# Optimization experiments

Measured on AMD Instinct MI355X. Metric: run time of the kernel, lower is better.

The kernel has to match this reference:

```python
import jax, jax.numpy as jnp
import numpy as np

N_NODES = 100000
N_EDGES = 1600000
EMBED = 64
HEADS = 8
HEAD_DIM = EMBED // HEADS
FFN = 4 * EMBED
EPS = 1e-5


def _layer_norm(x, g, b):
    m = jnp.mean(x, axis=-1, keepdims=True)
    v = jnp.mean(jnp.square(x - m), axis=-1, keepdims=True)
    return (x - m) * jax.lax.rsqrt(v + EPS) * g + b


def setup_inputs() -> dict:
    key = jax.random.key(0)
    ks = jax.random.split(key, 10)
    s = lambda fan_in: 1.0 / np.sqrt(fan_in)
    x = jax.random.normal(ks[0], (N_NODES, EMBED), dtype=jnp.float32)
    edge_indices = jax.random.randint(ks[1], (2, N_EDGES), 0, N_NODES, dtype=jnp.int64)
    attn_w = jax.random.uniform(ks[2], (EMBED, 3 * EMBED), jnp.float32, -s(EMBED), s(EMBED))
    attn_b = jnp.zeros((3 * EMBED,), jnp.float32)
    w1 = jax.random.uniform(ks[3], (EMBED, FFN), jnp.float32, -s(EMBED), s(EMBED))
    b1 = jnp.zeros((FFN,), jnp.float32)
    w2 = jax.random.uniform(ks[4], (FFN, EMBED), jnp.float32, -s(FFN), s(FFN))
    b2 = jnp.zeros((EMBED,), jnp.float32)
    ln1_g = jnp.ones((EMBED,), jnp.float32)
    ln1_b = jnp.zeros((EMBED,), jnp.float32)
    ln2_g = jnp.ones((EMBED,), jnp.float32)
    ln2_b = jnp.zeros((EMBED,), jnp.float32)
    return {"x": x, "edge_indices": edge_indices, "attn_w": attn_w, "attn_b": attn_b,
            "w1": w1, "b1": b1, "w2": w2, "b2": b2,
            "ln1_g": ln1_g, "ln1_b": ln1_b, "ln2_g": ln2_g, "ln2_b": ln2_b}


def _self_attention(x, edge_indices, attn_w, attn_b):
    n = x.shape[0]
    row, col = edge_indices[0], edge_indices[1]
    scale = EMBED ** (-0.5)  # note: original scales by embed_dim**-0.5
    qkv = (x @ attn_w + attn_b).reshape(n, HEADS, 3 * HEAD_DIM)
    q, k, v = jnp.split(qkv, 3, axis=2)  # each [N, H, Dh]
    alpha = jnp.sum(q[row] * k[col], axis=2) * scale  # [E, H]
    # sparse per-row softmax via segment reductions
    m = jax.ops.segment_max(alpha, row, num_segments=n)  # [N, H]
    e = jnp.exp(alpha - m[row])
    denom = jax.ops.segment_sum(e, row, num_segments=n)  # [N, H]
    weights = e / denom[row]  # [E, H]
    vals = v[col] * weights[:, :, None]  # [E, H, Dh]
    out = jax.ops.segment_sum(vals, row, num_segments=n)  # [N, H, Dh]
    return out.reshape(n, EMBED)


def reference(x, edge_indices, attn_w, attn_b, w1, b1, w2, b2, ln1_g, ln1_b, ln2_g, ln2_b):
    # post-norm (norm_first=False), dropout=0
    x = _layer_norm(x + _self_attention(x, edge_indices, attn_w, attn_b), ln1_g, ln1_b)
    ffn = jax.nn.relu(x @ w1 + b1) @ w2 + b2
    x = _layer_norm(x + ffn, ln2_g, ln2_b)
    return x
```

## Files before the change

kernel.cpp:

```cpp
#include <hip/hip_runtime.h>
#include <hip/hip_bf16.h>
#include <hip/hip_fp8.h>


#define WAVE 64
constexpr int BUCKET_SHIFT = 7;
constexpr int NBMAX = 800;

typedef __attribute__((ext_vector_type(8))) short bf16x8;
typedef __attribute__((ext_vector_type(4))) float f32x4;
typedef __attribute__((ext_vector_type(2))) float f32x2;

union BF8 {
  bf16x8 v;
  unsigned u[4];
};

__device__ __forceinline__ float bfbits_lo(unsigned u) {
  return __uint_as_float(u << 16);
}
__device__ __forceinline__ float bfbits_hi(unsigned u) {
  return __uint_as_float(u & 0xffff0000u);
}
__device__ __forceinline__ unsigned f2bf_pk(float a, float b) {
  unsigned ua = __float_as_uint(a);
  unsigned ub = __float_as_uint(b);
  ua = (ua + 0x7fff + ((ua >> 16) & 1)) >> 16;
  ub = (ub + 0x7fff + ((ub >> 16) & 1)) & 0xffff0000u;
  return ua | ub;
}
__device__ __forceinline__ unsigned short f2bf1(float a) {
  unsigned ua = __float_as_uint(a);
  ua = (ua + 0x7fff + ((ua >> 16) & 1)) >> 16;
  return (unsigned short)ua;
}

#if defined(__has_builtin)
#if __has_builtin(__builtin_amdgcn_cvt_pk_f32_fp8) && \
    __has_builtin(__builtin_amdgcn_cvt_pk_fp8_f32)
#define FP8_HW 1
#endif
#endif

#ifdef FP8_HW
#define FP8PK0(w) __builtin_amdgcn_cvt_pk_f32_fp8((int)(w), false)
#define FP8PK1(w) __builtin_amdgcn_cvt_pk_f32_fp8((int)(w), true)
__device__ __forceinline__ unsigned fp8enc4(float a, float b, float c,
                                            float d) {
  int r = __builtin_amdgcn_cvt_pk_fp8_f32(a, b, 0, false);
  r = __builtin_amdgcn_cvt_pk_fp8_f32(c, d, r, true);
  return (unsigned)r;
}
#else
__device__ __forceinline__ f32x2 fp8pk_sw(unsigned w, int sh) {
  __hip_fp8_e4m3 a, b;
  a.__x = (unsigned char)((w >> sh) & 0xff);
  b.__x = (unsigned char)((w >> (sh + 8)) & 0xff);
  f32x2 r;
  r.x = (float)a;
  r.y = (float)b;
  return r;
}
#define FP8PK0(w) fp8pk_sw((w), 0)
#define FP8PK1(w) fp8pk_sw((w), 16)
__device__ __forceinline__ unsigned fp8enc4(float a, float b, float c,
                                            float d) {
  __hip_fp8_e4m3 qa(a), qb(b), qc(c), qd(d);
  return (unsigned)qa.__x | ((unsigned)qb.__x << 8) |
         ((unsigned)qc.__x << 16) | ((unsigned)qd.__x << 24);
}
#endif

__device__ __forceinline__ float dot8_fp8(uint2 w, const float qv[8]) {
  f32x2 a = FP8PK0(w.x), b = FP8PK1(w.x), c = FP8PK0(w.y), d = FP8PK1(w.y);
  return a.x * qv[0] + a.y * qv[1] + b.x * qv[2] + b.y * qv[3] + c.x * qv[4] +
         c.y * qv[5] + d.x * qv[6] + d.y * qv[7];
}
__device__ __forceinline__ void acc8_fp8(uint2 w, float ee, float acc[8]) {
  f32x2 a = FP8PK0(w.x), b = FP8PK1(w.x), c = FP8PK0(w.y), d = FP8PK1(w.y);
  acc[0] += ee * a.x;
  acc[1] += ee * a.y;
  acc[2] += ee * b.x;
  acc[3] += ee * b.y;
  acc[4] += ee * c.x;
  acc[5] += ee * c.y;
  acc[6] += ee * d.x;
  acc[7] += ee * d.y;
}

__device__ __forceinline__ bool detect_is64_block(const int* __restrict__ e,
                                                  int* sflag) {
  if (threadIdx.x == 0) *sflag = 0;
  __syncthreads();
  unsigned v = 0;
  for (int i = threadIdx.x; i < 2048; i += blockDim.x)
    v |= (unsigned)e[2 * i + 1];
  if (v) atomicOr(sflag, 1);
  __syncthreads();
  return *sflag == 0;
}

__device__ __forceinline__ int edge_row(const int* e, int i, bool is64) {
  return is64 ? e[2 * (size_t)i] : e[i];
}
__device__ __forceinline__ int edge_col(const int* e, int i, int E, bool is64) {
  return is64 ? e[2 * ((size_t)E + i)] : e[(size_t)E + i];
}

__global__ __launch_bounds__(256) void cvt_w2(
    const float* __restrict__ aw, const float* __restrict__ w1,
    const float* __restrict__ w2, unsigned short* __restrict__ awT,
    unsigned short* __restrict__ w1T, unsigned short* __restrict__ w2T) {
  int tid = blockIdx.x * 256 + threadIdx.x;
  int stride = gridDim.x * 256;
  for (int i = tid; i < 192 * 64; i += stride) {
    int nn = i >> 6, kk = i & 63;
    awT[i] = f2bf1(aw[kk * 192 + nn]);
  }
  for (int i = tid; i < 256 * 64; i += stride) {
    int nn = i >> 6, kk = i & 63;
    w1T[i] = f2bf1(w1[kk * 256 + nn]);
  }
  for (int i = tid; i < 64 * 256; i += stride) {
    int nn = i >> 8, kk = i & 255;
    w2T[i] = f2bf1(w2[kk * 64 + nn]);
  }
}

__global__ __launch_bounds__(256) void bucket_count(const int* __restrict__ e,
                                                    int E,
                                                    int* __restrict__ tot,
                                                    int NB, int CH) {
  __shared__ int h[NBMAX];
  __shared__ int sflag;
  bool is64 = detect_is64_block(e, &sflag);
  for (int b = threadIdx.x; b < NB; b += 256) h[b] = 0;
  __syncthreads();
  int c0 = blockIdx.x * CH, c1 = min(E, c0 + CH);
  for (int i = c0 + threadIdx.x; i < c1; i += 256)
    atomicAdd(&h[edge_row(e, i, is64) >> BUCKET_SHIFT], 1);
  __syncthreads();
  for (int b = threadIdx.x; b < NB; b += 256)
    if (h[b]) atomicAdd(&tot[b], h[b]);
}

__global__ __launch_bounds__(1024) void scan_buckets(
    const int* __restrict__ tot, int NB, int* __restrict__ bucketstart,
    int* __restrict__ cursor) {
  __shared__ int wtot[16], wexcl[16];
  int tid = threadIdx.x;
  int lane = tid & 63, wid = tid >> 6;
  int v = (tid < NB) ? tot[tid] : 0;
  int incl = v;
#pragma unroll
  for (int m = 1; m < WAVE; m <<= 1) {
    int t = __shfl_up(incl, m);
    if (lane >= m) incl += t;
  }
  if (lane == 63) wtot[wid] = incl;
  __syncthreads();
  if (tid < 16) {
    int w = wtot[tid];
    int wi = w;
#pragma unroll
    for (int m = 1; m < 16; m <<= 1) {
      int t = __shfl_up(wi, m);
      if (tid >= m) wi += t;
    }
    wexcl[tid] = wi - w;
  }
  __syncthreads();
  int excl = wexcl[wid] + incl - v;
  if (tid < NB) {
    bucketstart[tid] = excl;
    cursor[tid] = excl;
  }
  if (tid == NB - 1) bucketstart[NB] = excl + v;
}

__global__ __launch_bounds__(256) void bucket_place(const int* __restrict__ e,
                                                    int E,
                                                    int* __restrict__ cursor,
                                                    unsigned* __restrict__ ebuf,
                                                    int NB, int CH) {
  __shared__ int cnt[NBMAX];
  __shared__ int sflag;
  bool is64 = detect_is64_block(e, &sflag);
  for (int b = threadIdx.x; b < NB; b += 256) cnt[b] = 0;
  __syncthreads();
  int c0 = blockIdx.x * CH, c1 = min(E, c0 + CH);
  for (int i = c0 + threadIdx.x; i < c1; i += 256)
    atomicAdd(&cnt[edge_row(e, i, is64) >> BUCKET_SHIFT], 1);
  __syncthreads();
  for (int b = threadIdx.x; b < NB; b += 256) {
    int c = cnt[b];
    cnt[b] = c ? atomicAdd(&cursor[b], c) : 0;
  }
  __syncthreads();
  for (int i = c0 + threadIdx.x; i < c1; i += 256) {
    int r = edge_row(e, i, is64);
    int c = edge_col(e, i, E, is64);
    int pos = atomicAdd(&cnt[r >> BUCKET_SHIFT], 1);
    ebuf[pos] = ((unsigned)(r & 127) << 17) | (unsigned)c;
  }
}

__global__ __launch_bounds__(256) void bucket_csr(
    const unsigned* __restrict__ ebuf, const int* __restrict__ bucketstart,
    int* __restrict__ ecol, int* __restrict__ rowstart, int n, int NB, int E) {
  __shared__ int cnt[128], offs[128], cur[128];
  const int b = blockIdx.x;
  const int tid = threadIdx.x;
  const int start = bucketstart[b];
  const int end = bucketstart[b + 1];
  if (tid < 128) cnt[tid] = 0;
  __syncthreads();
  for (int i = start + tid; i < end; i += 256)
    atomicAdd(&cnt[(ebuf[i] >> 17) & 127], 1);
  __syncthreads();
  if (tid < 128) offs[tid] = cnt[tid];
  __syncthreads();
  for (int s = 1; s < 128; s <<= 1) {
    int t = 0;
    if (tid < 128 && tid >= s) t = offs[tid - s];
    __syncthreads();
    if (tid < 128) offs[tid] += t;
    __syncthreads();
  }
  if (tid < 128) {
    int excl = offs[tid] - cnt[tid];
    cur[tid] = start + excl;
    int gr = (b << BUCKET_SHIFT) + tid;
    if (gr < n) rowstart[gr] = start + excl;
  }
  if (b == NB - 1 && tid == 0) rowstart[n] = E;
  __syncthreads();
  for (int i = start + tid; i < end; i += 256) {
    unsigned p = ebuf[i];
    int pos = atomicAdd(&cur[(p >> 17) & 127], 1);
    ecol[pos] = (int)(p & 0x1FFFF);
  }
}

template <int NCOLS, int K, int MODE, bool AFP32>
__global__ __launch_bounds__(256) void mfma_gemm(
    const void* __restrict__ A, const unsigned short* __restrict__ BT,
    const float* __restrict__ bias, unsigned short* __restrict__ out_q,
    unsigned char* __restrict__ out_kv8, unsigned short* __restrict__ out_h,
    const unsigned short* __restrict__ resid, const float* __restrict__ g,
    const float* __restrict__ beta, float* __restrict__ out_f, int n) {
  constexpr int KP = K + 8;
  constexpr int NT = NCOLS / 16;
  constexpr int NKC = K / 32;
  __shared__ unsigned short sB[NCOLS * KP];

  const int tid = threadIdx.x;
  {
    const uint4* src = (const uint4*)BT;
    for (int idx = tid; idx < NCOLS * K / 8; idx += 256) {
      int nn = idx / (K / 8), kq = idx % (K / 8);
      *(uint4*)&sB[nn * KP + kq * 8] = src[idx];
    }
  }
  __syncthreads();

  const int wid = tid >> 6, lane = tid & 63;
  const int l15 = lane & 15, quad = lane >> 4;
  const int rowbase = blockIdx.x * 128 + wid * 32;

  bf16x8 afrag[2][NKC];
#pragma unroll
  for (int rg = 0; rg < 2; rg++) {
    int row = rowbase + rg * 16 + l15;
    if (row >= n) row = n - 1;
    if (AFP32) {
      const float* Af = ((const float*)A) + (size_t)row * K;
#pragma unroll
      for (int kc = 0; kc < NKC; kc++) {
        float4 u0 = *(const float4*)(Af + kc * 32 + quad * 8);
        float4 u1 = *(const float4*)(Af + kc * 32 + quad * 8 + 4);
        BF8 t;
        t.u[0] = f2bf_pk(u0.x, u0.y);
        t.u[1] = f2bf_pk(u0.z, u0.w);
        t.u[2] = f2bf_pk(u1.x, u1.y);
        t.u[3] = f2bf_pk(u1.z, u1.w);
        afrag[rg][kc] = t.v;
      }
    } else {
      const bf16x8* ap = (const bf16x8*)((const unsigned short*)A + (size_t)row * K);
#pragma unroll
      for (int kc = 0; kc < NKC; kc++) afrag[rg][kc] = ap[kc * 4 + quad];
    }
  }

  f32x4 acc[2][NT];
#pragma unroll
  for (int rg = 0; rg < 2; rg++)
#pragma unroll
    for (int t = 0; t < NT; t++) acc[rg][t] = (f32x4){0.f, 0.f, 0.f, 0.f};

#pragma unroll
  for (int t = 0; t < NT; t++) {
#pragma unroll
    for (int kc = 0; kc < NKC; kc++) {
      bf16x8 b = *(const bf16x8*)&sB[(t * 16 + l15) * KP + kc * 32 + quad * 8];
      acc[0][t] = __builtin_amdgcn_mfma_f32_16x16x32_bf16(b, afrag[0][kc],
                                                          acc[0][t], 0, 0, 0);
      acc[1][t] = __builtin_amdgcn_mfma_f32_16x16x32_bf16(b, afrag[1][kc],
                                                          acc[1][t], 0, 0, 0);
    }
  }

  if (MODE == 0) {
#pragma unroll
    for (int rg = 0; rg < 2; rg++) {
      int row = rowbase + rg * 16 + l15;
      if (row >= n) continue;
#pragma unroll
      for (int t = 0; t < NT; t++) {
        int c0 = t * 16 + quad * 4;
        float4 bb = *(const float4*)&bias[c0];
        float v0 = acc[rg][t].x + bb.x, v1 = acc[rg][t].y + bb.y;
        float v2 = acc[rg][t].z + bb.z, v3 = acc[rg][t].w + bb.w;
        int hh = c0 / 24, rem = c0 % 24;
        if (rem < 8) {
          v0 *= 0.125f;
          v1 *= 0.125f;
          v2 *= 0.125f;
          v3 *= 0.125f;
          *(uint2*)(out_q + (size_t)row * 64 + hh * 8 + rem) =
              make_uint2(f2bf_pk(v0, v1), f2bf_pk(v2, v3));
        } else if (rem < 16) {
          *(unsigned*)(out_kv8 + (size_t)row * 128 + hh * 8 + (rem - 8)) =
              fp8enc4(v0, v1, v2, v3);
        } else {
          *(unsigned*)(out_kv8 + (size_t)row * 128 + 64 + hh * 8 + (rem - 16)) =
              fp8enc4(v0, v1, v2, v3);
        }
      }
    }
  } else if (MODE == 1) {
#pragma unroll
    for (int rg = 0; rg < 2; rg++) {
      int row = rowbase + rg * 16 + l15;
      if (row >= n) continue;
#pragma unroll
      for (int t = 0; t < NT; t++) {
        int c0 = t * 16 + quad * 4;
        float4 bb = *(const float4*)&bias[c0];
        float v0 = fmaxf(acc[rg][t].x + bb.x, 0.f);
        float v1 = fmaxf(acc[rg][t].y + bb.y, 0.f);
        float v2 = fmaxf(acc[rg][t].z + bb.z, 0.f);
        float v3 = fmaxf(acc[rg][t].w + bb.w, 0.f);
        *(uint2*)(out_h + (size_t)row * NCOLS + c0) =
            make_uint2(f2bf_pk(v0, v1), f2bf_pk(v2, v3));
      }
    }
  } else {
#pragma unroll
    for (int rg = 0; rg < 2; rg++) {
      int row = rowbase + rg * 16 + l15;
      bool ok = row < n;
      int rowc = ok ? row : n - 1;
      float vals[4][4];
      float ps = 0.f, pq = 0.f;
#pragma unroll
      for (int t = 0; t < 4; t++) {
        int c0 = t * 16 + quad * 4;
        float4 bb = *(const float4*)&bias[c0];
        uint2 rr = *(const uint2*)&resid[(size_t)rowc * 64 + c0];
        vals[t][0] = acc[rg][t].x + bb.x + bfbits_lo(rr.x);
        vals[t][1] = acc[rg][t].y + bb.y + bfbits_hi(rr.x);
        vals[t][2] = acc[rg][t].z + bb.z + bfbits_lo(rr.y);
        vals[t][3] = acc[rg][t].w + bb.w + bfbits_hi(rr.y);
#pragma unroll
        for (int r = 0; r < 4; r++) {
          ps += vals[t][r];
          pq += vals[t][r] * vals[t][r];
        }
      }
      ps += __shfl_xor(ps, 16);
      ps += __shfl_xor(ps, 32);
      pq += __shfl_xor(pq, 16);
      pq += __shfl_xor(pq, 32);
      float mean = ps * (1.f / 64.f);
      float var = pq * (1.f / 64.f) - mean * mean;
      float inv = rsqrtf(var + 1e-5f);
      if (ok) {
#pragma unroll
        for (int t = 0; t < 4; t++) {
          int c0 = t * 16 + quad * 4;
          float4 gg = *(const float4*)&g[c0];
          float4 be = *(const float4*)&beta[c0];
          float4 o = make_float4((vals[t][0] - mean) * inv * gg.x + be.x,
                                 (vals[t][1] - mean) * inv * gg.y + be.y,
                                 (vals[t][2] - mean) * inv * gg.z + be.z,
                                 (vals[t][3] - mean) * inv * gg.w + be.w);
          *(float4*)&out_f[(size_t)row * 64 + c0] = o;
        }
      }
    }
  }
}

__global__ __launch_bounds__(256) void attn_ln_kernel(
    const float* __restrict__ x, const unsigned short* __restrict__ qbuf,
    const unsigned char* __restrict__ kv8, const int* __restrict__ rowstart,
    const int* __restrict__ ecol, const float* __restrict__ g,
    const float* __restrict__ beta, unsigned short* __restrict__ x1b, int n) {
  int wave = threadIdx.x >> 6;
  int lane = threadIdx.x & 63;
  int node = blockIdx.x * 4 + wave;
  if (node >= n) return;
  const int e = lane >> 3, h = lane & 7;

  uint4 qp = ((const uint4*)(qbuf + (size_t)node * 64))[h];
  float qv[8] = {bfbits_lo(qp.x), bfbits_hi(qp.x), bfbits_lo(qp.y),
                 bfbits_hi(qp.y), bfbits_lo(qp.z), bfbits_hi(qp.z),
                 bfbits_lo(qp.w), bfbits_hi(qp.w)};

  int start = rowstart[node];
  int cnt = rowstart[node + 1] - start;
  float den = 0.f;
  float acc[8] = {0.f, 0.f, 0.f, 0.f, 0.f, 0.f, 0.f, 0.f};

  int iters = (cnt + 7) >> 3;
  int it = 0;
  for (; it + 2 <= iters; it += 2) {
    int i0 = it * 8 + e;
    int i1 = i0 + 8;
    bool v1 = i1 < cnt;
    int c0 = ecol[start + i0];
    int c1 = ecol[start + (v1 ? i1 : i0)];
    const unsigned char* r0 = kv8 + (size_t)c0 * 128 + h * 8;
    const unsigned char* r1 = kv8 + (size_t)c1 * 128 + h * 8;
    uint2 kw0 = *(const uint2*)r0;
    uint2 vw0 = *(const uint2*)(r0 + 64);
    uint2 kw1 = *(const uint2*)r1;
    uint2 vw1 = *(const uint2*)(r1 + 64);
    float a0 = dot8_fp8(kw0, qv);
    float a1 = dot8_fp8(kw1, qv);
    float e0 = __expf(a0);
    float e1 = v1 ? __expf(a1) : 0.f;
    den += e0 + e1;
    acc8_fp8(vw0, e0, acc);
    acc8_fp8(vw1, e1, acc);
  }
  if (it < iters) {
    int i0 = it * 8 + e;
    bool v0 = i0 < cnt;
    int c0 = ecol[start + (v0 ? i0 : 0)];
    const unsigned char* r0 = kv8 + (size_t)c0 * 128 + h * 8;
    uint2 kw0 = *(const uint2*)r0;
    uint2 vw0 = *(const uint2*)(r0 + 64);
    float a0 = dot8_fp8(kw0, qv);
    float e0 = v0 ? __expf(a0) : 0.f;
    den += e0;
    acc8_fp8(vw0, e0, acc);
  }

#pragma unroll
  for (int m = 8; m < 64; m <<= 1) {
    den += __shfl_xor(den, m);
#pragma unroll
    for (int j = 0; j < 8; j++) acc[j] += __shfl_xor(acc[j], m);
  }

  float invden = (cnt > 0) ? 1.f / den : 0.f;

  const float4* xr = (const float4*)(x + (size_t)node * 64 + h * 8);
  float4 xa = xr[0], xb4 = xr[1];
  float v[8];
  v[0] = xa.x + acc[0] * invden;
  v[1] = xa.y + acc[1] * invden;
  v[2] = xa.z + acc[2] * invden;
  v[3] = xa.w + acc[3] * invden;
  v[4] = xb4.x + acc[4] * invden;
  v[5] = xb4.y + acc[5] * invden;
  v[6] = xb4.z + acc[6] * invden;
  v[7] = xb4.w + acc[7] * invden;

  float ps = 0.f;
#pragma unroll
  for (int j = 0; j < 8; j++) ps += v[j];
#pragma unroll
  for (int m = 1; m < 8; m <<= 1) ps += __shfl_xor(ps, m);
  float mean = ps * (1.f / 64.f);
  float pq = 0.f;
#pragma unroll
  for (int j = 0; j < 8; j++) {
    float d = v[j] - mean;
    pq += d * d;
  }
#pragma unroll
  for (int m = 1; m < 8; m <<= 1) pq += __shfl_xor(pq, m);
  float inv = rsqrtf(pq * (1.f / 64.f) + 1e-5f);

  if (e == 0) {
    const float4* gr = (const float4*)(g + h * 8);
    const float4* br = (const float4*)(beta + h * 8);
    float4 ga = gr[0], gb = gr[1];
    float4 ba = br[0], bb = br[1];
    float o[8];
    o[0] = (v[0] - mean) * inv * ga.x + ba.x;
    o[1] = (v[1] - mean) * inv * ga.y + ba.y;
    o[2] = (v[2] - mean) * inv * ga.z + ba.z;
    o[3] = (v[3] - mean) * inv * ga.w + ba.w;
    o[4] = (v[4] - mean) * inv * gb.x + bb.x;
    o[5] = (v[5] - mean) * inv * gb.y + bb.y;
    o[6] = (v[6] - mean) * inv * gb.z + bb.z;
    o[7] = (v[7] - mean) * inv * gb.w + bb.w;
    *(uint4*)(x1b + (size_t)node * 64 + h * 8) =
        make_uint4(f2bf_pk(o[0], o[1]), f2bf_pk(o[2], o[3]),
                   f2bf_pk(o[4], o[5]), f2bf_pk(o[6], o[7]));
  }
}

extern "C" void kernel_launch(void* const* d_in, const int* in_sizes, int n_in,
                              void* d_out, int out_size, void* d_ws,
                              size_t ws_size, hipStream_t stream) {
  const float* x = (const float*)d_in[0];
  const int* edges = (const int*)d_in[1];
  const float* attn_w = (const float*)d_in[2];
  const float* attn_b = (const float*)d_in[3];
  const float* w1 = (const float*)d_in[4];
  const float* b1 = (const float*)d_in[5];
  const float* w2 = (const float*)d_in[6];
  const float* b2 = (const float*)d_in[7];
  const float* g1 = (const float*)d_in[8];
  const float* bb1 = (const float*)d_in[9];
  const float* g2 = (const float*)d_in[10];
  const float* bb2 = (const float*)d_in[11];

  const int N = in_sizes[0] / 64;
  const int E = in_sizes[1] / 2;
  const int NB = (N + 127) >> BUCKET_SHIFT;
  const int CH = (E + 255) / 256;

  char* ws = (char*)d_ws;
  size_t oq = 0;
  size_t okv = oq + (size_t)N * 128;
  size_t ox1b = okv + (size_t)N * 128;
  size_t oh = ox1b + (size_t)N * 128;
  size_t oawT = oh + (size_t)N * 512;
  size_t ow1T = oawT + 192 * 64 * 2;
  size_t ow2T = ow1T + 256 * 64 * 2;
  size_t oebuf = ow2T + 64 * 256 * 2;
  size_t oecol = oebuf + (size_t)E * 4;
  size_t orowstart = oecol + (size_t)E * 4;
  size_t otot = orowstart + (size_t)(N + 4) * 4;
  size_t obstart = otot + (size_t)(NBMAX) * 4;
  size_t ocursor = obstart + (size_t)(NBMAX + 4) * 4;

  unsigned short* qbuf = (unsigned short*)(ws + oq);
  unsigned char* kv8 = (unsigned char*)(ws + okv);
  unsigned short* x1b = (unsigned short*)(ws + ox1b);
  unsigned short* hbuf = (unsigned short*)(ws + oh);
  unsigned short* awT = (unsigned short*)(ws + oawT);
  unsigned short* w1T = (unsigned short*)(ws + ow1T);
  unsigned short* w2T = (unsigned short*)(ws + ow2T);
  unsigned* ebuf = (unsigned*)(ws + oebuf);
  int* ecol = (int*)(ws + oecol);
  int* rowstart = (int*)(ws + orowstart);
  int* tot = (int*)(ws + otot);
  int* bucketstart = (int*)(ws + obstart);
  int* cursor = (int*)(ws + ocursor);

  hipMemsetAsync(tot, 0, (size_t)NB * 4, stream);

  cvt_w2<<<32, 256, 0, stream>>>(attn_w, w1, w2, awT, w1T, w2T);

  bucket_count<<<256, 256, 0, stream>>>(edges, E, tot, NB, CH);
  scan_buckets<<<1, 1024, 0, stream>>>(tot, NB, bucketstart, cursor);
  bucket_place<<<256, 256, 0, stream>>>(edges, E, cursor, ebuf, NB, CH);
  bucket_csr<<<NB, 256, 0, stream>>>(ebuf, bucketstart, ecol, rowstart, N, NB,
                                     E);

  const int gblocks = (N + 127) / 128;

  mfma_gemm<192, 64, 0, true><<<gblocks, 256, 0, stream>>>(
      x, awT, attn_b, qbuf, kv8, nullptr, nullptr, nullptr, nullptr, nullptr,
      N);

  attn_ln_kernel<<<(N + 3) / 4, 256, 0, stream>>>(x, qbuf, kv8, rowstart, ecol,
                                                  g1, bb1, x1b, N);

  mfma_gemm<256, 64, 1, false><<<gblocks, 256, 0, stream>>>(
      x1b, w1T, b1, nullptr, nullptr, hbuf, nullptr, nullptr, nullptr, nullptr,
      N);

  mfma_gemm<64, 256, 2, false><<<gblocks, 256, 0, stream>>>(
      hbuf, w2T, b2, nullptr, nullptr, nullptr, x1b, g2, bb2, (float*)d_out,
      N);
}
```

Baseline: 284.0 us.

## Split QKV GEMM into dedicated kernel, pack fp8 attention math, fold memset

Moves the QKV projection into its own kernel, which reads weight fragments straight from global memory instead of staging them in LDS. Rewrites the attention dot and accumulate helpers to use two-wide float vectors so the compiler can emit packed FMA instructions. Folds the bucket-counter memset into the weight conversion kernel, which removes one API call. The risks are that global B loads in the QKV kernel may cost more than the LDS staging did, and that the packed math depends on the compiler actually vectorising it.

```diff
diff --git a/kernel.cpp b/kernel.cpp
--- a/kernel.cpp
+++ b/kernel.cpp
@@ -14,6 +14,7 @@
 union BF8 {
   bf16x8 v;
   unsigned u[4];
+  uint4 q;
 };
 
 __device__ __forceinline__ float bfbits_lo(unsigned u) {
@@ -71,21 +72,19 @@
 }
 #endif
 
-__device__ __forceinline__ float dot8_fp8(uint2 w, const float qv[8]) {
-  f32x2 a = FP8PK0(w.x), b = FP8PK1(w.x), c = FP8PK0(w.y), d = FP8PK1(w.y);
-  return a.x * qv[0] + a.y * qv[1] + b.x * qv[2] + b.y * qv[3] + c.x * qv[4] +
-         c.y * qv[5] + d.x * qv[6] + d.y * qv[7];
-}
-__device__ __forceinline__ void acc8_fp8(uint2 w, float ee, float acc[8]) {
-  f32x2 a = FP8PK0(w.x), b = FP8PK1(w.x), c = FP8PK0(w.y), d = FP8PK1(w.y);
-  acc[0] += ee * a.x;
-  acc[1] += ee * a.y;
-  acc[2] += ee * b.x;
-  acc[3] += ee * b.y;
-  acc[4] += ee * c.x;
-  acc[5] += ee * c.y;
-  acc[6] += ee * d.x;
-  acc[7] += ee * d.y;
+__device__ __forceinline__ float dot8_fp8_pk(uint2 w, const f32x2 qv2[4]) {
+  f32x2 s = FP8PK0(w.x) * qv2[0];
+  s += FP8PK1(w.x) * qv2[1];
+  s += FP8PK0(w.y) * qv2[2];
+  s += FP8PK1(w.y) * qv2[3];
+  return s.x + s.y;
+}
+__device__ __forceinline__ void acc8_fp8_pk(uint2 w, float ee, f32x2 acc2[4]) {
+  f32x2 e2 = {ee, ee};
+  acc2[0] += FP8PK0(w.x) * e2;
+  acc2[1] += FP8PK1(w.x) * e2;
+  acc2[2] += FP8PK0(w.y) * e2;
+  acc2[3] += FP8PK1(w.y) * e2;
 }
 
 __device__ __forceinline__ bool detect_is64_block(const int* __restrict__ e,
@@ -110,9 +109,11 @@
 __global__ __launch_bounds__(256) void cvt_w2(
     const float* __restrict__ aw, const float* __restrict__ w1,
     const float* __restrict__ w2, unsigned short* __restrict__ awT,
-    unsigned short* __restrict__ w1T, unsigned short* __restrict__ w2T) {
+    unsigned short* __restrict__ w1T, unsigned short* __restrict__ w2T,
+    int* __restrict__ tot, int NB) {
   int tid = blockIdx.x * 256 + threadIdx.x;
   int stride = gridDim.x * 256;
+  for (int i = tid; i < NB; i += stride) tot[i] = 0;
   for (int i = tid; i < 192 * 64; i += stride) {
     int nn = i >> 6, kk = i & 63;
     awT[i] = f2bf1(aw[kk * 192 + nn]);
@@ -242,11 +243,87 @@
   }
 }
 
-template <int NCOLS, int K, int MODE, bool AFP32>
+__global__ __launch_bounds__(256) void qkv_gemm(
+    const float* __restrict__ x, const unsigned short* __restrict__ awT,
+    const float* __restrict__ bias, unsigned short* __restrict__ qbuf,
+    unsigned char* __restrict__ kv8, int n) {
+  const int tid = threadIdx.x;
+  const int wid = tid >> 6, lane = tid & 63;
+  const int l15 = lane & 15, quad = lane >> 4;
+  const int rowbase = blockIdx.x * 128 + wid * 32;
+
+  bf16x8 afrag[2][2];
+#pragma unroll
+  for (int rg = 0; rg < 2; rg++) {
+    int row = rowbase + rg * 16 + l15;
+    int rowc = (row < n) ? row : n - 1;
+    const float* Af = x + (size_t)rowc * 64;
+#pragma unroll
+    for (int kc = 0; kc < 2; kc++) {
+      float4 u0 = *(const float4*)(Af + kc * 32 + quad * 8);
+      float4 u1 = *(const float4*)(Af + kc * 32 + quad * 8 + 4);
+      BF8 t;
+      t.u[0] = f2bf_pk(u0.x, u0.y);
+      t.u[1] = f2bf_pk(u0.z, u0.w);
+      t.u[2] = f2bf_pk(u1.x, u1.y);
+      t.u[3] = f2bf_pk(u1.z, u1.w);
+      afrag[rg][kc] = t.v;
+    }
+  }
+
+  f32x4 acc[2][12];
+#pragma unroll
+  for (int rg = 0; rg < 2; rg++)
+#pragma unroll
+    for (int t = 0; t < 12; t++) acc[rg][t] = (f32x4){0.f, 0.f, 0.f, 0.f};
+
+#pragma unroll
+  for (int t = 0; t < 12; t++) {
+#pragma unroll
+    for (int kc = 0; kc < 2; kc++) {
+      bf16x8 b =
+          *(const bf16x8*)(awT + (size_t)(t * 16 + l15) * 64 + kc * 32 +
+                           quad * 8);
+      acc[0][t] = __builtin_amdgcn_mfma_f32_16x16x32_bf16(b, afrag[0][kc],
+                                                          acc[0][t], 0, 0, 0);
+      acc[1][t] = __builtin_amdgcn_mfma_f32_16x16x32_bf16(b, afrag[1][kc],
+                                                          acc[1][t], 0, 0, 0);
+    }
+  }
+
+#pragma unroll
+  for (int rg = 0; rg < 2; rg++) {
+    int row = rowbase + rg * 16 + l15;
+    if (row >= n) continue;
+#pragma unroll
+    for (int t = 0; t < 12; t++) {
+      int c0 = t * 16 + quad * 4;
+      float4 bb = *(const float4*)&bias[c0];
+      float v0 = acc[rg][t].x + bb.x, v1 = acc[rg][t].y + bb.y;
+      float v2 = acc[rg][t].z + bb.z, v3 = acc[rg][t].w + bb.w;
+      int hh = c0 / 24, rem = c0 % 24;
+      if (rem < 8) {
+        v0 *= 0.125f;
+        v1 *= 0.125f;
+        v2 *= 0.125f;
+        v3 *= 0.125f;
+        *(uint2*)(qbuf + (size_t)row * 64 + hh * 8 + rem) =
+            make_uint2(f2bf_pk(v0, v1), f2bf_pk(v2, v3));
+      } else if (rem < 16) {
+        *(unsigned*)(kv8 + (size_t)row * 128 + hh * 8 + (rem - 8)) =
+            fp8enc4(v0, v1, v2, v3);
+      } else {
+        *(unsigned*)(kv8 + (size_t)row * 128 + 64 + hh * 8 + (rem - 16)) =
+            fp8enc4(v0, v1, v2, v3);
+      }
+    }
+  }
+}
+
+template <int NCOLS, int K, int MODE>
 __global__ __launch_bounds__(256) void mfma_gemm(
-    const void* __restrict__ A, const unsigned short* __restrict__ BT,
-    const float* __restrict__ bias, unsigned short* __restrict__ out_q,
-    unsigned char* __restrict__ out_kv8, unsigned short* __restrict__ out_h,
+    const unsigned short* __restrict__ A, const unsigned short* __restrict__ BT,
+    const float* __restrict__ bias, unsigned short* __restrict__ out_h,
     const unsigned short* __restrict__ resid, const float* __restrict__ g,
     const float* __restrict__ beta, float* __restrict__ out_f, int n) {
   constexpr int KP = K + 8;
@@ -273,24 +350,9 @@
   for (int rg = 0; rg < 2; rg++) {
     int row = rowbase + rg * 16 + l15;
     if (row >= n) row = n - 1;
-    if (AFP32) {
-      const float* Af = ((const float*)A) + (size_t)row * K;
-#pragma unroll
-      for (int kc = 0; kc < NKC; kc++) {
-        float4 u0 = *(const float4*)(Af + kc * 32 + quad * 8);
-        float4 u1 = *(const float4*)(Af + kc * 32 + quad * 8 + 4);
-        BF8 t;
-        t.u[0] = f2bf_pk(u0.x, u0.y);
-        t.u[1] = f2bf_pk(u0.z, u0.w);
-        t.u[2] = f2bf_pk(u1.x, u1.y);
-        t.u[3] = f2bf_pk(u1.z, u1.w);
-        afrag[rg][kc] = t.v;
-      }
-    } else {
-      const bf16x8* ap = (const bf16x8*)((const unsigned short*)A + (size_t)row * K);
-#pragma unroll
-      for (int kc = 0; kc < NKC; kc++) afrag[rg][kc] = ap[kc * 4 + quad];
-    }
+    const bf16x8* ap = (const bf16x8*)(A + (size_t)row * K);
+#pragma unroll
+    for (int kc = 0; kc < NKC; kc++) afrag[rg][kc] = ap[kc * 4 + quad];
   }
 
   f32x4 acc[2][NT];
@@ -311,35 +373,7 @@
     }
   }
 
-  if (MODE == 0) {
-#pragma unroll
-    for (int rg = 0; rg < 2; rg++) {
-      int row = rowbase + rg * 16 + l15;
-      if (row >= n) continue;
-#pragma unroll
-      for (int t = 0; t < NT; t++) {
-        int c0 = t * 16 + quad * 4;
-        float4 bb = *(const float4*)&bias[c0];
-        float v0 = acc[rg][t].x + bb.x, v1 = acc[rg][t].y + bb.y;
-        float v2 = acc[rg][t].z + bb.z, v3 = acc[rg][t].w + bb.w;
-        int hh = c0 / 24, rem = c0 % 24;
-        if (rem < 8) {
-          v0 *= 0.125f;
-          v1 *= 0.125f;
-          v2 *= 0.125f;
-          v3 *= 0.125f;
-          *(uint2*)(out_q + (size_t)row * 64 + hh * 8 + rem) =
-              make_uint2(f2bf_pk(v0, v1), f2bf_pk(v2, v3));
-        } else if (rem < 16) {
-          *(unsigned*)(out_kv8 + (size_t)row * 128 + hh * 8 + (rem - 8)) =
-              fp8enc4(v0, v1, v2, v3);
-        } else {
-          *(unsigned*)(out_kv8 + (size_t)row * 128 + 64 + hh * 8 + (rem - 16)) =
-              fp8enc4(v0, v1, v2, v3);
-        }
-      }
-    }
-  } else if (MODE == 1) {
+  if (MODE == 1) {
 #pragma unroll
     for (int rg = 0; rg < 2; rg++) {
       int row = rowbase + rg * 16 + l15;
@@ -415,14 +449,17 @@
   const int e = lane >> 3, h = lane & 7;
 
   uint4 qp = ((const uint4*)(qbuf + (size_t)node * 64))[h];
-  float qv[8] = {bfbits_lo(qp.x), bfbits_hi(qp.x), bfbits_lo(qp.y),
-                 bfbits_hi(qp.y), bfbits_lo(qp.z), bfbits_hi(qp.z),
-                 bfbits_lo(qp.w), bfbits_hi(qp.w)};
+  f32x2 qv2[4];
+  qv2[0] = (f32x2){bfbits_lo(qp.x), bfbits_hi(qp.x)};
+  qv2[1] = (f32x2){bfbits_lo(qp.y), bfbits_hi(qp.y)};
+  qv2[2] = (f32x2){bfbits_lo(qp.z), bfbits_hi(qp.z)};
+  qv2[3] = (f32x2){bfbits_lo(qp.w), bfbits_hi(qp.w)};
 
   int start = rowstart[node];
   int cnt = rowstart[node + 1] - start;
   float den = 0.f;
-  float acc[8] = {0.f, 0.f, 0.f, 0.f, 0.f, 0.f, 0.f, 0.f};
+  f32x2 acc2[4];
+  acc2[0] = acc2[1] = acc2[2] = acc2[3] = (f32x2){0.f, 0.f};
 
   int iters = (cnt + 7) >> 3;
   int it = 0;
@@ -438,13 +475,13 @@
     uint2 vw0 = *(const uint2*)(r0 + 64);
     uint2 kw1 = *(const uint2*)r1;
     uint2 vw1 = *(const uint2*)(r1 + 64);
-    float a0 = dot8_fp8(kw0, qv);
-    float a1 = dot8_fp8(kw1, qv);
+    float a0 = dot8_fp8_pk(kw0, qv2);
+    float a1 = dot8_fp8_pk(kw1, qv2);
     float e0 = __expf(a0);
     float e1 = v1 ? __expf(a1) : 0.f;
     den += e0 + e1;
-    acc8_fp8(vw0, e0, acc);
-    acc8_fp8(vw1, e1, acc);
+    acc8_fp8_pk(vw0, e0, acc2);
+    acc8_fp8_pk(vw1, e1, acc2);
   }
   if (it < iters) {
     int i0 = it * 8 + e;
@@ -453,17 +490,20 @@
     const unsigned char* r0 = kv8 + (size_t)c0 * 128 + h * 8;
     uint2 kw0 = *(const uint2*)r0;
     uint2 vw0 = *(const uint2*)(r0 + 64);
-    float a0 = dot8_fp8(kw0, qv);
+    float a0 = dot8_fp8_pk(kw0, qv2);
     float e0 = v0 ? __expf(a0) : 0.f;
     den += e0;
-    acc8_fp8(vw0, e0, acc);
+    acc8_fp8_pk(vw0, e0, acc2);
   }
 
 #pragma unroll
   for (int m = 8; m < 64; m <<= 1) {
     den += __shfl_xor(den, m);
 #pragma unroll
-    for (int j = 0; j < 8; j++) acc[j] += __shfl_xor(acc[j], m);
+    for (int j = 0; j < 4; j++) {
+      acc2[j].x += __shfl_xor(acc2[j].x, m);
+      acc2[j].y += __shfl_xor(acc2[j].y, m);
+    }
   }
 
   float invden = (cnt > 0) ? 1.f / den : 0.f;
@@ -471,14 +511,14 @@
   const float4* xr = (const float4*)(x + (size_t)node * 64 + h * 8);
   float4 xa = xr[0], xb4 = xr[1];
   float v[8];
-  v[0] = xa.x + acc[0] * invden;
-  v[1] = xa.y + acc[1] * invden;
-  v[2] = xa.z + acc[2] * invden;
-  v[3] = xa.w + acc[3] * invden;
-  v[4] = xb4.x + acc[4] * invden;
-  v[5] = xb4.y + acc[5] * invden;
-  v[6] = xb4.z + acc[6] * invden;
-  v[7] = xb4.w + acc[7] * invden;
+  v[0] = xa.x + acc2[0].x * invden;
+  v[1] = xa.y + acc2[0].y * invden;
+  v[2] = xa.z + acc2[1].x * invden;
+  v[3] = xa.w + acc2[1].y * invden;
+  v[4] = xb4.x + acc2[2].x * invden;
+  v[5] = xb4.y + acc2[2].y * invden;
+  v[6] = xb4.z + acc2[3].x * invden;
+  v[7] = xb4.w + acc2[3].y * invden;
 
   float ps = 0.f;
 #pragma unroll
@@ -566,9 +606,7 @@
   int* bucketstart = (int*)(ws + obstart);
   int* cursor = (int*)(ws + ocursor);
 
-  hipMemsetAsync(tot, 0, (size_t)NB * 4, stream);
-
-  cvt_w2<<<32, 256, 0, stream>>>(attn_w, w1, w2, awT, w1T, w2T);
+  cvt_w2<<<32, 256, 0, stream>>>(attn_w, w1, w2, awT, w1T, w2T, tot, NB);
 
   bucket_count<<<256, 256, 0, stream>>>(edges, E, tot, NB, CH);
   scan_buckets<<<1, 1024, 0, stream>>>(tot, NB, bucketstart, cursor);
@@ -578,18 +616,14 @@
 
   const int gblocks = (N + 127) / 128;
 
-  mfma_gemm<192, 64, 0, true><<<gblocks, 256, 0, stream>>>(
-      x, awT, attn_b, qbuf, kv8, nullptr, nullptr, nullptr, nullptr, nullptr,
-      N);
+  qkv_gemm<<<gblocks, 256, 0, stream>>>(x, awT, attn_b, qbuf, kv8, N);
 
   attn_ln_kernel<<<(N + 3) / 4, 256, 0, stream>>>(x, qbuf, kv8, rowstart, ecol,
                                                   g1, bb1, x1b, N);
 
-  mfma_gemm<256, 64, 1, false><<<gblocks, 256, 0, stream>>>(
-      x1b, w1T, b1, nullptr, nullptr, hbuf, nullptr, nullptr, nullptr, nullptr,
-      N);
-
-  mfma_gemm<64, 256, 2, false><<<gblocks, 256, 0, stream>>>(
-      hbuf, w2T, b2, nullptr, nullptr, nullptr, x1b, g2, bb2, (float*)d_out,
-      N);
-}
+  mfma_gemm<256, 64, 1><<<gblocks, 256, 0, stream>>>(
+      x1b, w1T, b1, hbuf, nullptr, nullptr, nullptr, nullptr, N);
+
+  mfma_gemm<64, 256, 2><<<gblocks, 256, 0, stream>>>(
+      hbuf, w2T, b2, nullptr, x1b, g2, bb2, (float*)d_out, N);
+}
```

New measurement: 287.6 us. No clear change (+1.3%).
